# Kernel optimization log

Hardware: AMD Instinct MI355X
Metric: run time of the kernel (lower is better)

The kernel has to match this reference:

```python
import jax, jax.numpy as jnp
import numpy as np


def setup_inputs() -> dict:
    key = jax.random.key(0)
    ks = jax.random.split(key, 8)
    B, dz, K, N, dx, T = 64, 16, 16, 1024, 128, 500
    # initial latent state [n_trials, dz, k_particles]
    z0 = jax.random.normal(ks[0], (B, dz, K), jnp.float32)
    # per-latent leak/time-constant A = (1 - dt/tau), kept in (0.8, 0.99) for stability
    A = jax.random.uniform(ks[1], (dz,), jnp.float32, minval=0.8, maxval=0.99)
    # low-rank recurrent factors: n [dz, N] (right), m [N, dz] (left)
    n = jax.random.normal(ks[2], (dz, N), jnp.float32) * (1.0 / N)
    m = jax.random.normal(ks[3], (N, dz), jnp.float32) * (1.0 / np.sqrt(dz))
    # neuron bias h [N], latent bias hz [dz]
    h = jax.random.normal(ks[4], (N,), jnp.float32) * 0.1
    hz = jax.random.normal(ks[5], (dz,), jnp.float32) * 0.01
    # readout B [dz, dx] ~ sqrt(2/dy) randn, bias initialised to zero (as in Observation)
    Bobs = jax.random.normal(ks[6], (dz, dx), jnp.float32) * np.sqrt(2.0 / dz)
    Bias = jnp.zeros((dx,), jnp.float32)
    return {"z0": z0, "A": A, "n": n, "m": m, "h": h, "hz": hz,
            "Bobs": Bobs, "Bias": Bias, "T": T}


def reference(z0, A, n, m, h, hz, Bobs, Bias, T):
    """Low-rank RNN rolled out for T steps + linear (identity-nonlin) readout.

    Per step (Transition.forward with relu nonlinearity, weight_scaler=1, du=0):
        R   = relu(m @ z - h)                       # rates, [B, N, K]
        z'  = A * z + n @ R + hz                    # [B, dz, K]
    Readout (Observation.forward, identity nonlinearity):
        X = einsum('zx,bzTK->bxTK', Bobs, zs) + Bias
    """
    Ab = A[None, :, None]      # [1, dz, 1]
    hb = h[None, :, None]      # [1, N, 1]
    hzb = hz[None, :, None]    # [1, dz, 1]

    def step(z, _):
        X = jnp.einsum('Nz,bzk->bNk', m, z)           # project to neurons
        R = jax.nn.relu(X - hb)                       # rates
        z_new = Ab * z + jnp.einsum('zN,bNk->bzk', n, R) + hzb
        return z_new, z_new

    _, zs = jax.lax.scan(step, z0, None, length=T)    # [T, B, dz, K]
    zs = jnp.transpose(zs, (1, 2, 0, 3))              # [B, dz, T, K]
    # Observation readout
    X = jnp.einsum('zx,bzTK->bxTK', Bobs, zs) + Bias[None, :, None, None]
    return X
```

## Files before the change

### kernel.cpp

```cpp
#include <hip/hip_runtime.h>
#include <hip/hip_bf16.h>


typedef __attribute__((ext_vector_type(4))) short short4v;
typedef __attribute__((ext_vector_type(8))) short short8v;
typedef __attribute__((ext_vector_type(4))) float float4v;

#define BB 64
#define DZ 16
#define KC 16
#define NN 1024
#define DX 128
#define NW 4
#define ITER (NN / (16 * NW))
#define NH (ITER / 2)
#define NT (DX / (16 * NW))
#define CH 8

union FragAB {
  short4v s;
  __hip_bfloat162 h2[2];
};
union Frag8 {
  short8v s8;
  short4v s4[2];
};

__device__ inline short4v pack_bf16x4(float a, float b, float c, float d) {
  FragAB u;
  u.h2[0] = __float22bfloat162_rn(make_float2(a, b));
  u.h2[1] = __float22bfloat162_rn(make_float2(c, d));
  return u.s;
}

__device__ inline float4v mfma_bf16(short4v a, short4v b, float4v c) {
#if __has_builtin(__builtin_amdgcn_mfma_f32_16x16x16bf16_1k)
  return __builtin_amdgcn_mfma_f32_16x16x16bf16_1k(a, b, c, 0, 0, 0);
#elif __has_builtin(__builtin_amdgcn_mfma_f32_16x16x16_bf16)
  return __builtin_amdgcn_mfma_f32_16x16x16_bf16(a, b, c, 0, 0, 0);
#else
  float4v d;
  asm("v_mfma_f32_16x16x16_bf16 %0, %1, %2, %3"
      : "=v"(d) : "v"(a), "v"(b), "v"(c));
  return d;
#endif
}

__device__ inline float4v mfma_bf16_x32(short8v a, short8v b, float4v c) {
#if __has_builtin(__builtin_amdgcn_mfma_f32_16x16x32_bf16)
  return __builtin_amdgcn_mfma_f32_16x16x32_bf16(a, b, c, 0, 0, 0);
#else
  float4v d;
  asm("v_mfma_f32_16x16x32_bf16 %0, %1, %2, %3"
      : "=v"(d) : "v"(a), "v"(b), "v"(c));
  return d;
#endif
}

__global__ __launch_bounds__(64 * NW, 1)
void lrrnn_fused(const float* __restrict__ z0, const float* __restrict__ Adec,
                 const float* __restrict__ nmat, const float* __restrict__ mmat,
                 const float* __restrict__ hvec, const float* __restrict__ hzvec,
                 const float* __restrict__ Bobs, const float* __restrict__ Bias,
                 const int* __restrict__ Tptr, float* __restrict__ out)
{
  const int T    = Tptr[0];
  const int b    = blockIdx.x;
  const int tid  = threadIdx.x;
  const int wave = tid >> 6;
  const int lane = tid & 63;
  const int g    = lane >> 4;
  const int c    = lane & 15;

  __shared__ float4v part[2][NW][64];

  FragAB mf[ITER];
  Frag8  nf8[NH];
  float4v negH[ITER];
#pragma unroll
  for (int i = 0; i < ITER; ++i) {
    const int rowbase = wave * (16 * ITER) + i * 16;
    float4v mv = *(const float4v*)(mmat + (rowbase + c) * DZ + g * 4);
    mf[i].s = pack_bf16x4(mv[0], mv[1], mv[2], mv[3]);
    float4v hv = *(const float4v*)(hvec + rowbase + g * 4);
    negH[i][0] = -hv[0]; negH[i][1] = -hv[1];
    negH[i][2] = -hv[2]; negH[i][3] = -hv[3];
  }
#pragma unroll
  for (int i = 0; i < NH; ++i) {
    const int rb0 = wave * (16 * ITER) + (2 * i) * 16;
    float4v nv0 = *(const float4v*)(nmat + c * NN + rb0 + g * 4);
    float4v nv1 = *(const float4v*)(nmat + c * NN + rb0 + 16 + g * 4);
    nf8[i].s4[0] = pack_bf16x4(nv0[0], nv0[1], nv0[2], nv0[3]);
    nf8[i].s4[1] = pack_bf16x4(nv1[0], nv1[1], nv1[2], nv1[3]);
  }

  const float4v Af  = *(const float4v*)(Adec + g * 4);
  const float4v hzf = *(const float4v*)(hzvec + g * 4);
  const float4v zerov = {0.f, 0.f, 0.f, 0.f};

  FragAB bobsF[NT];
  float4v biasF[NT];
  unsigned oof[NT][4];
#pragma unroll
  for (int s = 0; s < NT; ++s) {
    const int xb = (wave * NT + s) * 16;
    bobsF[s].s = pack_bf16x4(Bobs[(4 * g + 0) * DX + xb + c],
                             Bobs[(4 * g + 1) * DX + xb + c],
                             Bobs[(4 * g + 2) * DX + xb + c],
                             Bobs[(4 * g + 3) * DX + xb + c]);
    biasF[s] = *(const float4v*)(Bias + xb + g * 4);
#pragma unroll
    for (int rr = 0; rr < 4; ++rr) {
      const int x = xb + g * 4 + rr;
      oof[s][rr] = (unsigned)(b * DX + x) * (unsigned)T * KC + c;
    }
  }

  float4v zf;
#pragma unroll
  for (int j = 0; j < 4; ++j)
    zf[j] = z0[b * DZ * KC + (g * 4 + j) * KC + c];
  FragAB zb;
  zb.s = pack_bf16x4(zf[0], zf[1], zf[2], zf[3]);

  auto do_step = [&](int buf) {
    float4v az;
#pragma unroll
    for (int j = 0; j < 4; ++j)
      az[j] = fmaf(Af[j], zf[j], hzf[j]);

    float4v acc[4] = {zerov, zerov, zerov, zerov};
#pragma unroll
    for (int grp = 0; grp < 2; ++grp) {
      float4v xv[8];
#pragma unroll
      for (int i = 0; i < 8; ++i)
        xv[i] = mfma_bf16(mf[grp * 8 + i].s, zb.s, negH[grp * 8 + i]);
      Frag8 R8[4];
#pragma unroll
      for (int i = 0; i < 4; ++i) {
        const float4v x0 = xv[2 * i], x1 = xv[2 * i + 1];
        R8[i].s4[0] = pack_bf16x4(fmaxf(x0[0], 0.f), fmaxf(x0[1], 0.f),
                                  fmaxf(x0[2], 0.f), fmaxf(x0[3], 0.f));
        R8[i].s4[1] = pack_bf16x4(fmaxf(x1[0], 0.f), fmaxf(x1[1], 0.f),
                                  fmaxf(x1[2], 0.f), fmaxf(x1[3], 0.f));
      }
      acc[grp * 2 + 0] = mfma_bf16_x32(nf8[grp * 4 + 0].s8, R8[0].s8, acc[grp * 2 + 0]);
      acc[grp * 2 + 1] = mfma_bf16_x32(nf8[grp * 4 + 1].s8, R8[1].s8, acc[grp * 2 + 1]);
      acc[grp * 2 + 0] = mfma_bf16_x32(nf8[grp * 4 + 2].s8, R8[2].s8, acc[grp * 2 + 0]);
      acc[grp * 2 + 1] = mfma_bf16_x32(nf8[grp * 4 + 3].s8, R8[3].s8, acc[grp * 2 + 1]);
    }
    const float4v zp = (acc[0] + acc[1]) + (acc[2] + acc[3]);

    part[buf][wave][lane] = zp;
    __syncthreads();

    const float4v p0 = part[buf][0][lane];
    const float4v p1 = part[buf][1][lane];
    const float4v p2 = part[buf][2][lane];
    const float4v p3 = part[buf][3][lane];
    const float4v tot = (p0 + p1) + (p2 + p3);
#pragma unroll
    for (int j = 0; j < 4; ++j)
      zf[j] = az[j] + tot[j];
    zb.s = pack_bf16x4(zf[0], zf[1], zf[2], zf[3]);
  };

  int t = 0;
  while (t + CH <= T) {
    short4v hist[CH];
#pragma unroll
    for (int s = 0; s < CH; ++s) {
      do_step(s & 1);
      hist[s] = zb.s;
    }
#pragma unroll
    for (int s = 0; s < CH; ++s) {
#pragma unroll
      for (int q = 0; q < NT; ++q) {
        float4v o = mfma_bf16(bobsF[q].s, hist[s], biasF[q]);
        const unsigned tk = (unsigned)(t + s) * KC;
#pragma unroll
        for (int rr = 0; rr < 4; ++rr)
          out[oof[q][rr] + tk] = o[rr];
      }
    }
    t += CH;
  }
  for (; t < T; ++t) {
    do_step(t & 1);
#pragma unroll
    for (int q = 0; q < NT; ++q) {
      float4v o = mfma_bf16(bobsF[q].s, zb.s, biasF[q]);
      const unsigned tk = (unsigned)t * KC;
#pragma unroll
      for (int rr = 0; rr < 4; ++rr)
        out[oof[q][rr] + tk] = o[rr];
    }
  }
}

extern "C" void kernel_launch(void* const* d_in, const int* in_sizes, int n_in,
                              void* d_out, int out_size, void* d_ws, size_t ws_size,
                              hipStream_t stream) {
  const float* z0   = (const float*)d_in[0];
  const float* A    = (const float*)d_in[1];
  const float* nmat = (const float*)d_in[2];
  const float* mmat = (const float*)d_in[3];
  const float* h    = (const float*)d_in[4];
  const float* hz   = (const float*)d_in[5];
  const float* Bobs = (const float*)d_in[6];
  const float* Bias = (const float*)d_in[7];
  const int*   T    = (const int*)d_in[8];
  (void)in_sizes; (void)n_in; (void)out_size; (void)d_ws; (void)ws_size;
  lrrnn_fused<<<dim3(BB), dim3(64 * NW), 0, stream>>>(
      z0, A, nmat, mmat, h, hz, Bobs, Bias, T, (float*)d_out);
}
```

Measured before the change: 393.4 us.

## Halve waves per block to cut cross-wave reduction and barrier cost

Drops the block from four waves to two, so each wave handles twice as many neurons per step and the LDS partial-sum reduction reads only two partials. The per-step __syncthreads is replaced with an explicit lgkmcnt wait plus s_barrier, and the leak update is folded into a single fma after the barrier. The output address precompute is simplified to one base per tile using a row stride. The cost is more serial MFMA work per wave and fewer waves to hide latency on the sequential recurrence.

```diff
diff --git a/kernel.cpp b/kernel.cpp
--- a/kernel.cpp
+++ b/kernel.cpp
@@ -11,11 +11,13 @@
 #define KC 16
 #define NN 1024
 #define DX 128
-#define NW 4
+#define NW 2
 #define ITER (NN / (16 * NW))
 #define NH (ITER / 2)
 #define NT (DX / (16 * NW))
 #define CH 8
+
+#define BARRIER_LGKM() asm volatile("s_waitcnt lgkmcnt(0)\n\ts_barrier" ::: "memory")
 
 union FragAB {
   short4v s;
@@ -36,8 +38,6 @@
 __device__ inline float4v mfma_bf16(short4v a, short4v b, float4v c) {
 #if __has_builtin(__builtin_amdgcn_mfma_f32_16x16x16bf16_1k)
   return __builtin_amdgcn_mfma_f32_16x16x16bf16_1k(a, b, c, 0, 0, 0);
-#elif __has_builtin(__builtin_amdgcn_mfma_f32_16x16x16_bf16)
-  return __builtin_amdgcn_mfma_f32_16x16x16_bf16(a, b, c, 0, 0, 0);
 #else
   float4v d;
   asm("v_mfma_f32_16x16x16_bf16 %0, %1, %2, %3"
@@ -88,7 +88,7 @@
   }
 #pragma unroll
   for (int i = 0; i < NH; ++i) {
-    const int rb0 = wave * (16 * ITER) + (2 * i) * 16;
+    const int rb0 = wave * (16 * ITER) + i * 32;
     float4v nv0 = *(const float4v*)(nmat + c * NN + rb0 + g * 4);
     float4v nv1 = *(const float4v*)(nmat + c * NN + rb0 + 16 + g * 4);
     nf8[i].s4[0] = pack_bf16x4(nv0[0], nv0[1], nv0[2], nv0[3]);
@@ -101,20 +101,17 @@
 
   FragAB bobsF[NT];
   float4v biasF[NT];
-  unsigned oof[NT][4];
-#pragma unroll
-  for (int s = 0; s < NT; ++s) {
-    const int xb = (wave * NT + s) * 16;
-    bobsF[s].s = pack_bf16x4(Bobs[(4 * g + 0) * DX + xb + c],
+  unsigned oofq[NT];
+  const unsigned rstride = (unsigned)T * KC;
+#pragma unroll
+  for (int q = 0; q < NT; ++q) {
+    const int xb = (wave * NT + q) * 16;
+    bobsF[q].s = pack_bf16x4(Bobs[(4 * g + 0) * DX + xb + c],
                              Bobs[(4 * g + 1) * DX + xb + c],
                              Bobs[(4 * g + 2) * DX + xb + c],
                              Bobs[(4 * g + 3) * DX + xb + c]);
-    biasF[s] = *(const float4v*)(Bias + xb + g * 4);
-#pragma unroll
-    for (int rr = 0; rr < 4; ++rr) {
-      const int x = xb + g * 4 + rr;
-      oof[s][rr] = (unsigned)(b * DX + x) * (unsigned)T * KC + c;
-    }
+    biasF[q] = *(const float4v*)(Bias + xb + g * 4);
+    oofq[q] = (unsigned)(b * DX + xb + g * 4) * rstride + c;
   }
 
   float4v zf;
@@ -125,45 +122,36 @@
   zb.s = pack_bf16x4(zf[0], zf[1], zf[2], zf[3]);
 
   auto do_step = [&](int buf) {
-    float4v az;
-#pragma unroll
-    for (int j = 0; j < 4; ++j)
-      az[j] = fmaf(Af[j], zf[j], hzf[j]);
-
     float4v acc[4] = {zerov, zerov, zerov, zerov};
 #pragma unroll
-    for (int grp = 0; grp < 2; ++grp) {
+    for (int grp = 0; grp < 4; ++grp) {
       float4v xv[8];
 #pragma unroll
-      for (int i = 0; i < 8; ++i)
-        xv[i] = mfma_bf16(mf[grp * 8 + i].s, zb.s, negH[grp * 8 + i]);
+      for (int j = 0; j < 8; ++j)
+        xv[j] = mfma_bf16(mf[grp * 8 + j].s, zb.s, negH[grp * 8 + j]);
       Frag8 R8[4];
 #pragma unroll
-      for (int i = 0; i < 4; ++i) {
-        const float4v x0 = xv[2 * i], x1 = xv[2 * i + 1];
-        R8[i].s4[0] = pack_bf16x4(fmaxf(x0[0], 0.f), fmaxf(x0[1], 0.f),
-                                  fmaxf(x0[2], 0.f), fmaxf(x0[3], 0.f));
-        R8[i].s4[1] = pack_bf16x4(fmaxf(x1[0], 0.f), fmaxf(x1[1], 0.f),
-                                  fmaxf(x1[2], 0.f), fmaxf(x1[3], 0.f));
+      for (int jj = 0; jj < 4; ++jj) {
+        const float4v x0 = xv[2 * jj], x1 = xv[2 * jj + 1];
+        R8[jj].s4[0] = pack_bf16x4(fmaxf(x0[0], 0.f), fmaxf(x0[1], 0.f),
+                                   fmaxf(x0[2], 0.f), fmaxf(x0[3], 0.f));
+        R8[jj].s4[1] = pack_bf16x4(fmaxf(x1[0], 0.f), fmaxf(x1[1], 0.f),
+                                   fmaxf(x1[2], 0.f), fmaxf(x1[3], 0.f));
       }
-      acc[grp * 2 + 0] = mfma_bf16_x32(nf8[grp * 4 + 0].s8, R8[0].s8, acc[grp * 2 + 0]);
-      acc[grp * 2 + 1] = mfma_bf16_x32(nf8[grp * 4 + 1].s8, R8[1].s8, acc[grp * 2 + 1]);
-      acc[grp * 2 + 0] = mfma_bf16_x32(nf8[grp * 4 + 2].s8, R8[2].s8, acc[grp * 2 + 0]);
-      acc[grp * 2 + 1] = mfma_bf16_x32(nf8[grp * 4 + 3].s8, R8[3].s8, acc[grp * 2 + 1]);
+#pragma unroll
+      for (int jj = 0; jj < 4; ++jj)
+        acc[jj] = mfma_bf16_x32(nf8[grp * 4 + jj].s8, R8[jj].s8, acc[jj]);
     }
     const float4v zp = (acc[0] + acc[1]) + (acc[2] + acc[3]);
 
     part[buf][wave][lane] = zp;
-    __syncthreads();
+    BARRIER_LGKM();
 
     const float4v p0 = part[buf][0][lane];
     const float4v p1 = part[buf][1][lane];
-    const float4v p2 = part[buf][2][lane];
-    const float4v p3 = part[buf][3][lane];
-    const float4v tot = (p0 + p1) + (p2 + p3);
 #pragma unroll
     for (int j = 0; j < 4; ++j)
-      zf[j] = az[j] + tot[j];
+      zf[j] = fmaf(Af[j], zf[j], (p0[j] + p1[j]) + hzf[j]);
     zb.s = pack_bf16x4(zf[0], zf[1], zf[2], zf[3]);
   };
 
@@ -172,18 +160,18 @@
     short4v hist[CH];
 #pragma unroll
     for (int s = 0; s < CH; ++s) {
-      do_step(s & 1);
+      do_step((t + s) & 1);
       hist[s] = zb.s;
     }
 #pragma unroll
-    for (int s = 0; s < CH; ++s) {
-#pragma unroll
-      for (int q = 0; q < NT; ++q) {
+    for (int q = 0; q < NT; ++q) {
+#pragma unroll
+      for (int s = 0; s < CH; ++s) {
         float4v o = mfma_bf16(bobsF[q].s, hist[s], biasF[q]);
-        const unsigned tk = (unsigned)(t + s) * KC;
+        const unsigned base = oofq[q] + (unsigned)(t + s) * KC;
 #pragma unroll
         for (int rr = 0; rr < 4; ++rr)
-          out[oof[q][rr] + tk] = o[rr];
+          out[base + rr * rstride] = o[rr];
       }
     }
     t += CH;
@@ -193,10 +181,10 @@
 #pragma unroll
     for (int q = 0; q < NT; ++q) {
       float4v o = mfma_bf16(bobsF[q].s, zb.s, biasF[q]);
-      const unsigned tk = (unsigned)t * KC;
+      const unsigned base = oofq[q] + (unsigned)t * KC;
 #pragma unroll
       for (int rr = 0; rr < 4; ++rr)
-        out[oof[q][rr] + tk] = o[rr];
+        out[base + rr * rstride] = o[rr];
     }
   }
 }
```

Result: slower. 682.6 us (+73.5%).
